# Optimization experiments

Hardware: AMD Instinct MI355X
Metric: run time of the kernel (lower is better)

Reference implementation:

```python
import jax, jax.numpy as jnp
import numpy as np
from math import pi

IN_CH = 32
OUT_CH = 32
ORIENT = 8
K = 5  # kernel_size (kor == kh == kw == K)


def _b2(t):
    # Quadratic (order-2) cardinal B-spline, matching lietorch.bspline order=2.
    a = jnp.abs(t)
    return jnp.where(a <= 0.5, 0.75 - a * a,
                     jnp.where(a < 1.5, 0.5 * (1.5 - a) ** 2, 0.0))


def _kernel_stack(weights):
    # nodes: Cartesian grid of control points, identical for every (out,in) pair
    off = (K - 1) / 2.0
    xs = jnp.linspace(-off, off, K)
    og, yg, xg = jnp.meshgrid(xs, xs, xs, indexing='ij')
    nodes = jnp.stack([og, yg, xg], axis=-1).reshape(-1, 3)  # [K^3, 3]
    # rotated M2 Cartesian grid stack [O, K, K, K, 3] (order, y, x)
    angles = -jnp.arange(ORIENT, dtype=jnp.float32) * (2.0 * pi / ORIENT)
    c = jnp.cos(angles)[:, None, None, None]
    s = jnp.sin(angles)[:, None, None, None]
    xr = xg * c + yg * s
    yr = -xg * s + yg * c
    org = jnp.broadcast_to(og, xr.shape)
    grid = jnp.stack([org, yr, xr], axis=-1)  # [O, K, K, K, 3]
    # B-spline sampling (scales == 1): tensor-product basis, then weighted sum
    diff = grid[..., None, :] - nodes  # [O, K, K, K, K^3, 3]
    basis = _b2(diff).prod(axis=-1)    # [O, K, K, K, K^3]
    # kernel_stack [Cout, Cin, O, K, K, K]
    return jnp.einsum('uvn,oabcn->uvoabc', weights, basis)


def setup_inputs() -> dict:
    key = jax.random.key(0)
    k1, k2 = jax.random.split(key)
    x = jax.random.normal(k1, (8, IN_CH, ORIENT, 128, 128), dtype=jnp.float32)
    # xavier_normal_ with relu gain, fan based on [Cout, Cin, K^3]
    gain = np.sqrt(2.0)
    std = np.float32(gain * np.sqrt(2.0 / (IN_CH * K ** 3 + OUT_CH * K ** 3)))
    weights = std * jax.random.normal(k2, (OUT_CH, IN_CH, K ** 3), dtype=jnp.float32)
    return {"x": x, "weights": weights}


def reference(x, weights):
    # x: [B, Cin, O, H, W]
    ks = _kernel_stack(weights)  # [Cout, Cin, O, K, K, K]
    pb = (K - 1 + 1) // 2  # ceil((kor-1)/2)
    pt = (K - 1) // 2      # floor((kor-1)/2)
    xp = jnp.pad(x, ((0, 0), (0, 0), (pb, pt), (0, 0), (0, 0)), mode='wrap')
    dn = ('NCDHW', 'OIDHW', 'NCDHW')
    outs = [
        jax.lax.conv_general_dilated(
            jax.lax.dynamic_slice_in_dim(xp, i, K, axis=2),
            ks[:, :, i],
            window_strides=(1, 1, 1),
            padding='VALID',
            dimension_numbers=dn,
        )  # [B, Cout, 1, H-K+1, W-K+1]
        for i in range(ORIENT)
    ]
    return jnp.concatenate(outs, axis=2)  # [B, Cout, O, H-K+1, W-K+1]
```

## Files before the change

### kernel.cpp

```cpp
#include <hip/hip_runtime.h>
#include <stdint.h>


typedef _Float16 half8 __attribute__((ext_vector_type(8)));
typedef float f32x4 __attribute__((ext_vector_type(4)));

#define HOUT 124
#define KSF_B 67108864ULL
#define WT_B 69156864ULL
#define BAS_B 69668864ULL
#define WS_NEED 70168864ULL

#define AS1(p) ((const __attribute__((address_space(1))) void*)(p))
#define AS3(p) ((__attribute__((address_space(3))) void*)(p))

__device__ __forceinline__ float b2f(float t) {
  float a = fabsf(t);
  if (a <= 0.5f) return 0.75f - a * a;
  if (a < 1.5f) { float u = 1.5f - a; return 0.5f * u * u; }
  return 0.0f;
}


__global__ __launch_bounds__(256) void wt_kernel(const float* __restrict__ w,
                                                 float* __restrict__ wT) {
  __shared__ float lw[4000];
  const int co = blockIdx.x;
  for (int i = threadIdx.x; i < 4000; i += 256) lw[i] = w[(size_t)co * 4000 + i];
  __syncthreads();
  for (int i = threadIdx.x; i < 4000; i += 256) {
    const int n = i >> 5, ci = i & 31;
    wT[(size_t)n * 1024 + co * 32 + ci] = lw[ci * 125 + n];
  }
}

__global__ __launch_bounds__(256) void basis_kernel(float* __restrict__ bas) {
  const int blk = blockIdx.x;
  const int o = blk / 25, ko = (blk / 5) % 5, ky = blk % 5;
  const float ang = -(float)o * 0.78539816339744830962f;
  const float c0 = cosf(ang), s0 = sinf(ang);
  for (int i = threadIdx.x; i < 625; i += 256) {
    const int kx = i / 125, node = i - kx * 125;
    const int no = node / 25, ny = (node / 5) % 5, nx = node % 5;
    const float gy = (float)(ky - 2), gx = (float)(kx - 2);
    const float xr = gx * c0 + gy * s0;
    const float yr = -gx * s0 + gy * c0;
    bas[(size_t)blk * 625 + i] = b2f((float)(ko - no)) *
                                 b2f(yr - (float)(ny - 2)) *
                                 b2f(xr - (float)(nx - 2));
  }
}

__global__ __launch_bounds__(256) void build_ks_fast(
    const float* __restrict__ wT, const float* __restrict__ bas,
    _Float16* __restrict__ ksf) {
  const int blk = blockIdx.x;
  const int tapblk = blk >> 1, cot = blk & 1;
  const float* bp = bas + (size_t)tapblk * 625;
  const float* w0 = wT + cot * 512 + threadIdx.x;
  float s0_[5] = {0, 0, 0, 0, 0}, s1_[5] = {0, 0, 0, 0, 0};
  #pragma unroll 5
  for (int n = 0; n < 125; ++n) {
    const float a = w0[(size_t)n * 1024];
    const float b = w0[(size_t)n * 1024 + 256];
    #pragma unroll
    for (int kx = 0; kx < 5; ++kx) {
      const float bb = bp[kx * 125 + n];
      s0_[kx] = fmaf(a, bb, s0_[kx]);
      s1_[kx] = fmaf(b, bb, s1_[kx]);
    }
  }
  #pragma unroll
  for (int pi = 0; pi < 2; ++pi) {
    const int pr = threadIdx.x + pi * 256;
    const int co = cot * 16 + (pr >> 5), ci = pr & 31;
    const int l = ((ci >> 3) << 4) | (co & 15), jj = ci & 7;
    const float* sv = pi ? s1_ : s0_;
    #pragma unroll
    for (int kx = 0; kx < 5; ++kx)
      ksf[((size_t)(tapblk * 5 + kx) * 2 + cot) * 512 + l * 8 + jj] =
          (_Float16)sv[kx];
  }
}

__global__ __launch_bounds__(256) void xh_kernel(const float* __restrict__ x,
                                                 _Float16* __restrict__ xh) {
  __shared__ float lx[32][128];
  const int blk = blockIdx.x;
  const int plane = blk >> 7, y = blk & 127;
  const int b_ = plane >> 3, j = plane & 7;
  const int t = threadIdx.x;
  const int ci0 = t >> 5, px0 = (t & 31) * 4;
  #pragma unroll
  for (int p = 0; p < 4; ++p) {
    const int ci = p * 8 + ci0;
    const float4 v = *(const float4*)(
        x + ((size_t)((b_ * 32 + ci) * 8 + j) << 14) + (y << 7) + px0);
    *(float4*)&lx[ci][px0] = v;
  }
  __syncthreads();
  const int px = t >> 1, q0 = (t & 1) * 2;
  const int key = (px >> 1) & 3;
  union { _Float16 h[16]; uint4 u[2]; } v;
  #pragma unroll
  for (int qi = 0; qi < 2; ++qi) {
    const int cib = ((q0 + qi) ^ key) * 8;
    #pragma unroll
    for (int r = 0; r < 8; ++r) v.h[qi * 8 + r] = (_Float16)lx[cib + r][px];
  }
  uint4* dst = (uint4*)(xh + ((size_t)plane << 19) + ((size_t)y << 12) +
                        px * 32 + q0 * 8);
  dst[0] = v.u[0];
  dst[1] = v.u[1];
}

__global__ __launch_bounds__(512, 2) void conv_fast(
    const _Float16* __restrict__ xh, const _Float16* __restrict__ ksf,
    float* __restrict__ out) {
  __shared__ __align__(16) char tile[12 * 128 * 64 + 256];
  const int bid = blockIdx.x;
  const int b_ = bid >> 7;
  const int rem = bid & 127;
  const int o = rem >> 4;
  const int y0 = (rem & 15) * 8;
  const int t = threadIdx.x;
  const int wv = t >> 6;
  const int l = t & 63;
  const int lg = l >> 4;
  const int ln = l & 15;

  f32x4 acc[8][2];
  #pragma unroll
  for (int s = 0; s < 8; ++s) {
    acc[s][0] = (f32x4)0.0f;
    acc[s][1] = (f32x4)0.0f;
  }

  #pragma unroll 1
  for (int ko = 0; ko < 5; ++ko) {
    const int j = (o + ko + 6) & 7;
    const char* src = (const char*)xh + ((size_t)(b_ * 8 + j) << 20) +
                      ((size_t)y0 << 13);
    __syncthreads();
    #pragma unroll
    for (int i = 0; i < 12; ++i) {
      const int c = wv * 12 + i;
      __builtin_amdgcn_global_load_lds(AS1(src + c * 1024 + l * 16),
                                       AS3(tile + c * 1024), 16, 0, 0);
    }
    asm volatile("s_waitcnt vmcnt(0)");
    __syncthreads();
    #pragma unroll
    for (int ky = 0; ky < 5; ++ky) {
      const _Float16* kbase =
          ksf + (size_t)(((o * 5 + ko) * 5 + ky) * 5) * 1024 + l * 8;
      half8 af[5][2];
      #pragma unroll
      for (int kx = 0; kx < 5; ++kx) {
        af[kx][0] = *(const half8*)(kbase + (size_t)(kx * 2 + 0) * 512);
        af[kx][1] = *(const half8*)(kbase + (size_t)(kx * 2 + 1) * 512);
      }
      const int rb = (wv + ky) * 128 + ln;
      #pragma unroll
      for (int s = 0; s < 8; ++s) {
        #pragma unroll
        for (int kx = 0; kx < 5; ++kx) {
          const int pixel = rb + s * 16 + kx;
          const half8 bx = *(const half8*)(
              tile + pixel * 64 + ((lg ^ ((pixel >> 1) & 3)) << 4));
          acc[s][0] = __builtin_amdgcn_mfma_f32_16x16x32_f16(af[kx][0], bx,
                                                             acc[s][0], 0, 0, 0);
          acc[s][1] = __builtin_amdgcn_mfma_f32_16x16x32_f16(af[kx][1], bx,
                                                             acc[s][1], 0, 0, 0);
        }
      }
    }
  }

  const int y = y0 + wv;
  if (y < HOUT) {
    #pragma unroll
    for (int s = 0; s < 8; ++s) {
      const int px = s * 16 + ln;
      if (px < HOUT) {
        #pragma unroll
        for (int cot = 0; cot < 2; ++cot) {
          #pragma unroll
          for (int r = 0; r < 4; ++r) {
            const int co = cot * 16 + lg * 4 + r;
            out[(size_t)((b_ * 32 + co) * 8 + o) * (HOUT * HOUT) + y * HOUT +
                px] = acc[s][cot][r];
          }
        }
      }
    }
  }
}


__global__ __launch_bounds__(256) void build_ks(const float* __restrict__ w,
                                                _Float16* __restrict__ ksf) {
  __shared__ float basis[5 * 125];
  const int blk = blockIdx.x;
  const int o = blk / 25, ko = (blk / 5) % 5, ky = blk % 5;
  const float ang = -(float)o * 0.78539816339744830962f;
  const float c0 = cosf(ang), s0 = sinf(ang);
  for (int i = threadIdx.x; i < 625; i += 256) {
    const int kx = i / 125, node = i - kx * 125;
    const int no = node / 25, ny = (node / 5) % 5, nx = node % 5;
    const float gy = (float)(ky - 2), gx = (float)(kx - 2);
    const float xr = gx * c0 + gy * s0;
    const float yr = -gx * s0 + gy * c0;
    basis[i] = b2f((float)(ko - no)) * b2f(yr - (float)(ny - 2)) *
               b2f(xr - (float)(nx - 2));
  }
  __syncthreads();
  #pragma unroll 1
  for (int p = 0; p < 20; ++p) {
    const int e = threadIdx.x + p * 256;
    const int jj = e & 7, l = (e >> 3) & 63, cot = (e >> 9) & 1, kx = e >> 10;
    const int co = cot * 16 + (l & 15);
    const int ci = ((l >> 4) & 3) * 8 + jj;
    const float* wp = w + (size_t)(co * 32 + ci) * 125;
    const float* bp = basis + kx * 125;
    float s = 0.0f;
    #pragma unroll 5
    for (int n = 0; n < 125; ++n) s = fmaf(wp[n], bp[n], s);
    ksf[((size_t)(blk * 5 + kx) * 2 + cot) * 512 + l * 8 + jj] = (_Float16)s;
  }
}

#define TW 132
__global__ __launch_bounds__(512, 2) void conv_mfma(
    const float* __restrict__ x, const _Float16* __restrict__ ksf,
    float* __restrict__ out) {
  __shared__ __align__(16) char tile[12 * TW * 64];
  const int bid = blockIdx.x;
  const int b_ = bid >> 7;
  const int rem = bid & 127;
  const int o = rem >> 4;
  const int y0 = (rem & 15) * 8;
  const int t = threadIdx.x;
  const int wv = t >> 6;
  const int l = t & 63;
  const int lg = l >> 4;
  const int ln = l & 15;

  f32x4 acc[8][2];
  #pragma unroll
  for (int s = 0; s < 8; ++s) {
    acc[s][0] = (f32x4)0.0f;
    acc[s][1] = (f32x4)0.0f;
  }
  const float* xb = x + (size_t)b_ * (32u * 8u * 128u * 128u);

  #pragma unroll 1
  for (int ko = 0; ko < 5; ++ko) {
    const int j = (o + ko + 6) & 7;
    __syncthreads();
    #pragma unroll 1
    for (int task = wv; task < 384; task += 8) {
      const int cb = task & 3;
      const int pb = (task >> 2) & 7;
      const int r = task >> 5;
      const int c2 = cb * 4 + lg;
      const int px = pb * 16 + ln;
      int row = y0 + r;
      if (row > 127) row = 127;
      const float* g0 = xb + (size_t)(2 * c2) * (8 * 128 * 128) +
                        (size_t)j * (128 * 128) + row * 128 + px;
      const float f0 = g0[0];
      const float f1 = g0[8 * 128 * 128];
      union { _Float16 h[2]; unsigned u; } cv;
      cv.h[0] = (_Float16)f0;
      cv.h[1] = (_Float16)f1;
      const int pixel = r * TW + px;
      *(unsigned*)(tile + pixel * 64 +
                   (((c2 >> 2) ^ ((pixel >> 1) & 3)) << 4) +
                   ((c2 & 3) << 2)) = cv.u;
    }
    __syncthreads();
    #pragma unroll 1
    for (int ky = 0; ky < 5; ++ky) {
      const _Float16* kbase =
          ksf + (size_t)(((o * 5 + ko) * 5 + ky) * 5) * 1024 + l * 8;
      half8 af[5][2];
      #pragma unroll
      for (int kx = 0; kx < 5; ++kx) {
        af[kx][0] = *(const half8*)(kbase + (size_t)(kx * 2 + 0) * 512);
        af[kx][1] = *(const half8*)(kbase + (size_t)(kx * 2 + 1) * 512);
      }
      const int rbase = (wv + ky) * TW + ln;
      #pragma unroll
      for (int s = 0; s < 8; ++s) {
        #pragma unroll
        for (int kx = 0; kx < 5; ++kx) {
          const int pixel = rbase + s * 16 + kx;
          const half8 bx = *(const half8*)(
              tile + pixel * 64 + ((lg ^ ((pixel >> 1) & 3)) << 4));
          acc[s][0] = __builtin_amdgcn_mfma_f32_16x16x32_f16(af[kx][0], bx,
                                                             acc[s][0], 0, 0, 0);
          acc[s][1] = __builtin_amdgcn_mfma_f32_16x16x32_f16(af[kx][1], bx,
                                                             acc[s][1], 0, 0, 0);
        }
      }
    }
  }

  const int y = y0 + wv;
  if (y < HOUT) {
    #pragma unroll
    for (int s = 0; s < 8; ++s) {
      const int px = s * 16 + ln;
      if (px < HOUT) {
        #pragma unroll
        for (int cot = 0; cot < 2; ++cot) {
          #pragma unroll
          for (int r = 0; r < 4; ++r) {
            const int co = cot * 16 + lg * 4 + r;
            out[(size_t)((b_ * 32 + co) * 8 + o) * (HOUT * HOUT) + y * HOUT +
                px] = acc[s][cot][r];
          }
        }
      }
    }
  }
}

extern "C" void kernel_launch(void* const* d_in, const int* in_sizes, int n_in,
                              void* d_out, int out_size, void* d_ws, size_t ws_size,
                              hipStream_t stream) {
  const float* x = (const float*)d_in[0];
  const float* w = (const float*)d_in[1];
  float* out = (float*)d_out;
  if (ws_size >= WS_NEED) {
    _Float16* xh = (_Float16*)d_ws;
    _Float16* ksf = (_Float16*)((char*)d_ws + KSF_B);
    float* wT = (float*)((char*)d_ws + WT_B);
    float* bas = (float*)((char*)d_ws + BAS_B);
    hipLaunchKernelGGL(wt_kernel, dim3(32), dim3(256), 0, stream, w, wT);
    hipLaunchKernelGGL(basis_kernel, dim3(200), dim3(256), 0, stream, bas);
    hipLaunchKernelGGL(build_ks_fast, dim3(400), dim3(256), 0, stream, wT, bas, ksf);
    hipLaunchKernelGGL(xh_kernel, dim3(8192), dim3(256), 0, stream, x, xh);
    hipLaunchKernelGGL(conv_fast, dim3(1024), dim3(512), 0, stream, xh, ksf, out);
  } else {
    _Float16* ksf = (_Float16*)d_ws;
    hipLaunchKernelGGL(build_ks, dim3(200), dim3(256), 0, stream, w, ksf);
    hipLaunchKernelGGL(conv_mfma, dim3(1024), dim3(512), 0, stream, x, ksf, out);
  }
}
```

Measured before the change: 677.3 us.

## Double-buffer input tiles and split each row across two waves in conv kernel

Replaces the conv kernel with a version that prefetches the next orientation slice into a second LDS buffer while the current one feeds the MFMAs. The block tile shrinks from 8 rows to 4 rows, with two waves per row each handling half the pixel columns, and the grid grows from 1024 to 1984 blocks. This halves accumulator registers per wave and cuts wasted rows past the 124-row edge. The cost is more blocks re-reading overlapping halo rows, and launch bounds drop to one block per CU with 128KB of LDS.

```diff
diff --git a/kernel.cpp b/kernel.cpp
--- a/kernel.cpp
+++ b/kernel.cpp
@@ -114,42 +114,60 @@
   dst[1] = v.u[1];
 }
 
-__global__ __launch_bounds__(512, 2) void conv_fast(
+__global__ __launch_bounds__(512, 1) void conv_fast2(
     const _Float16* __restrict__ xh, const _Float16* __restrict__ ksf,
     float* __restrict__ out) {
-  __shared__ __align__(16) char tile[12 * 128 * 64 + 256];
+  __shared__ __align__(16) char tile[2][8 * 128 * 64];
   const int bid = blockIdx.x;
-  const int b_ = bid >> 7;
-  const int rem = bid & 127;
-  const int o = rem >> 4;
-  const int y0 = (rem & 15) * 8;
+  const int b_ = bid / 248;
+  const int rem = bid - b_ * 248;
+  const int o = rem / 31;
+  const int y0 = (rem - o * 31) * 4;
   const int t = threadIdx.x;
   const int wv = t >> 6;
   const int l = t & 63;
   const int lg = l >> 4;
   const int ln = l & 15;
-
-  f32x4 acc[8][2];
-  #pragma unroll
-  for (int s = 0; s < 8; ++s) {
+  const int row = wv >> 1;
+  const int h = wv & 1;
+
+  f32x4 acc[4][2];
+  #pragma unroll
+  for (int s = 0; s < 4; ++s) {
     acc[s][0] = (f32x4)0.0f;
     acc[s][1] = (f32x4)0.0f;
   }
 
+  const char* xbase = (const char*)xh + ((size_t)b_ << 23);
+
+  {
+    const int j0 = (o + 6) & 7;
+    const char* src = xbase + ((size_t)j0 << 20) + ((size_t)y0 << 13);
+    #pragma unroll
+    for (int i = 0; i < 8; ++i) {
+      const int c = wv * 8 + i;
+      __builtin_amdgcn_global_load_lds(AS1(src + c * 1024 + l * 16),
+                                       AS3(tile[0] + c * 1024), 16, 0, 0);
+    }
+  }
+
   #pragma unroll 1
   for (int ko = 0; ko < 5; ++ko) {
-    const int j = (o + ko + 6) & 7;
-    const char* src = (const char*)xh + ((size_t)(b_ * 8 + j) << 20) +
-                      ((size_t)y0 << 13);
+    asm volatile("s_waitcnt vmcnt(0)" ::: "memory");
     __syncthreads();
-    #pragma unroll
-    for (int i = 0; i < 12; ++i) {
-      const int c = wv * 12 + i;
-      __builtin_amdgcn_global_load_lds(AS1(src + c * 1024 + l * 16),
-                                       AS3(tile + c * 1024), 16, 0, 0);
-    }
-    asm volatile("s_waitcnt vmcnt(0)");
-    __syncthreads();
+    if (ko < 4) {
+      const int jn = (o + ko + 7) & 7;
+      const char* src = xbase + ((size_t)jn << 20) + ((size_t)y0 << 13);
+      char* dstb = tile[(ko + 1) & 1];
+      #pragma unroll
+      for (int i = 0; i < 8; ++i) {
+        const int c = wv * 8 + i;
+        __builtin_amdgcn_global_load_lds(AS1(src + c * 1024 + l * 16),
+                                         AS3(dstb + c * 1024), 16, 0, 0);
+      }
+    }
+    __builtin_amdgcn_sched_barrier(0);
+    const char* tb = tile[ko & 1];
     #pragma unroll
     for (int ky = 0; ky < 5; ++ky) {
       const _Float16* kbase =
@@ -160,14 +178,14 @@
         af[kx][0] = *(const half8*)(kbase + (size_t)(kx * 2 + 0) * 512);
         af[kx][1] = *(const half8*)(kbase + (size_t)(kx * 2 + 1) * 512);
       }
-      const int rb = (wv + ky) * 128 + ln;
-      #pragma unroll
-      for (int s = 0; s < 8; ++s) {
+      const int rb = (row + ky) * 128 + ln;
+      #pragma unroll
+      for (int s = 0; s < 4; ++s) {
         #pragma unroll
         for (int kx = 0; kx < 5; ++kx) {
-          const int pixel = rb + s * 16 + kx;
+          const int pixel = rb + (h * 4 + s) * 16 + kx;
           const half8 bx = *(const half8*)(
-              tile + pixel * 64 + ((lg ^ ((pixel >> 1) & 3)) << 4));
+              tb + pixel * 64 + ((lg ^ ((pixel >> 1) & 3)) << 4));
           acc[s][0] = __builtin_amdgcn_mfma_f32_16x16x32_f16(af[kx][0], bx,
                                                              acc[s][0], 0, 0, 0);
           acc[s][1] = __builtin_amdgcn_mfma_f32_16x16x32_f16(af[kx][1], bx,
@@ -177,20 +195,18 @@
     }
   }
 
-  const int y = y0 + wv;
-  if (y < HOUT) {
-    #pragma unroll
-    for (int s = 0; s < 8; ++s) {
-      const int px = s * 16 + ln;
-      if (px < HOUT) {
+  const int y = y0 + row;
+  #pragma unroll
+  for (int s = 0; s < 4; ++s) {
+    const int px = (h * 4 + s) * 16 + ln;
+    if (px < HOUT) {
+      #pragma unroll
+      for (int cot = 0; cot < 2; ++cot) {
         #pragma unroll
-        for (int cot = 0; cot < 2; ++cot) {
-          #pragma unroll
-          for (int r = 0; r < 4; ++r) {
-            const int co = cot * 16 + lg * 4 + r;
-            out[(size_t)((b_ * 32 + co) * 8 + o) * (HOUT * HOUT) + y * HOUT +
-                px] = acc[s][cot][r];
-          }
+        for (int r = 0; r < 4; ++r) {
+          const int co = cot * 16 + lg * 4 + r;
+          out[(size_t)((b_ * 32 + co) * 8 + o) * (HOUT * HOUT) + y * HOUT +
+              px] = acc[s][cot][r];
         }
       }
     }
@@ -342,7 +358,7 @@
     hipLaunchKernelGGL(basis_kernel, dim3(200), dim3(256), 0, stream, bas);
     hipLaunchKernelGGL(build_ks_fast, dim3(400), dim3(256), 0, stream, wT, bas, ksf);
     hipLaunchKernelGGL(xh_kernel, dim3(8192), dim3(256), 0, stream, x, xh);
-    hipLaunchKernelGGL(conv_fast, dim3(1024), dim3(512), 0, stream, xh, ksf, out);
+    hipLaunchKernelGGL(conv_fast2, dim3(1984), dim3(512), 0, stream, xh, ksf, out);
   } else {
     _Float16* ksf = (_Float16*)d_ws;
     hipLaunchKernelGGL(build_ks, dim3(200), dim3(256), 0, stream, w, ksf);
```

After: 569.6 us. 15.9% less time.
